# Performance work log

Hardware: AMD Instinct MI355X
Metric: run time of the kernel (lower is better)

The kernel has to match this reference:

```python
import jax, jax.numpy as jnp
import numpy as np

E = 1024      # emb_dim
H = 16        # num_heads
DH = E // H   # per-head atten_dim
B = 2
T = 2048


def _layernorm(x, scale, shift, eps=1e-5):
    mean = x.mean(axis=-1, keepdims=True)
    var = ((x - mean) ** 2).mean(axis=-1, keepdims=True)  # unbiased=False
    return scale * (x - mean) / jnp.sqrt(var + eps) + shift


def _gelu(x):
    # Faithful to source: tanh(sqrt(2/pi)*x + 0.044715*x^3)  (no sqrt on cubic term)
    c = jnp.sqrt(jnp.asarray(2.0 / jnp.pi, x.dtype))
    return 0.5 * x * (1.0 + jnp.tanh(c * x + 0.044715 * x ** 3))


def setup_inputs() -> dict:
    key = jax.random.key(0)
    ks = jax.random.split(key, 12)
    s = 0.02
    return {
        "x":     jax.random.normal(ks[0], (B, T, E), jnp.float32),
        "Wq":    jax.random.normal(ks[1], (H, E, DH), jnp.float32) * s,
        "Wk":    jax.random.normal(ks[2], (H, E, DH), jnp.float32) * s,
        "Wv":    jax.random.normal(ks[3], (H, E, DH), jnp.float32) * s,
        "fc_w":  jax.random.normal(ks[4], (E, E), jnp.float32) * s,
        "fc_b":  jnp.zeros((E,), jnp.float32),
        "ln1_s": jnp.ones((E,), jnp.float32),
        "ln1_b": jnp.zeros((E,), jnp.float32),
        "ln2_s": jnp.ones((E,), jnp.float32),
        "ln2_b": jnp.zeros((E,), jnp.float32),
        "ff_w1": jax.random.normal(ks[5], (E, 4 * E), jnp.float32) * s,
        "ff_b1": jnp.zeros((4 * E,), jnp.float32),
        "ff_w2": jax.random.normal(ks[6], (4 * E, E), jnp.float32) * s,
        "ff_b2": jnp.zeros((E,), jnp.float32),
    }


def _attention(x, Wq, Wk, Wv, fc_w, fc_b):
    b, t, _ = x.shape
    q = jnp.einsum("bte,hed->bhtd", x, Wq)
    k = jnp.einsum("bte,hed->bhtd", x, Wk)
    v = jnp.einsum("bte,hed->bhtd", x, Wv)
    scores = jnp.einsum("bhtd,bhsd->bhts", q, k)
    causal = jnp.triu(jnp.ones((t, t), bool), 1)
    scores = jnp.where(causal, -jnp.inf, scores)
    w = jax.nn.softmax(scores / jnp.sqrt(jnp.asarray(DH, x.dtype)), axis=-1)
    ctx = jnp.einsum("bhts,bhsd->bhtd", w, v)
    # faithful quirk from source: per-head transpose(1,2) then reshape(b, T, d_out)
    ctx = jnp.swapaxes(ctx, 2, 3).reshape(b, H, t, DH)
    concat = ctx.transpose(0, 2, 1, 3).reshape(b, t, E)
    return concat @ fc_w + fc_b


def reference(x, Wq, Wk, Wv, fc_w, fc_b, ln1_s, ln1_b, ln2_s, ln2_b,
              ff_w1, ff_b1, ff_w2, ff_b2):
    h = _attention(_layernorm(x, ln1_s, ln1_b), Wq, Wk, Wv, fc_w, fc_b) + x
    y = _layernorm(h, ln2_s, ln2_b)
    y = _gelu(y @ ff_w1 + ff_b1) @ ff_w2 + ff_b2
    return y + h
```

## Files before the change

### kernel.cpp

```cpp
#include <hip/hip_runtime.h>


#define En 1024
#define Hn 16
#define DHn 64
#define Bn 2
#define Tn 2048
#define Mrows 4096

typedef __attribute__((ext_vector_type(8))) short bf16x8;
typedef __attribute__((ext_vector_type(4))) float f32x4;

__device__ __forceinline__ short f2bf(float f) {
    unsigned u = __float_as_uint(f);
    u += 0x7FFFu + ((u >> 16) & 1u);
    return (short)(u >> 16);
}
__device__ __forceinline__ ushort f2bfu(float f) {
    unsigned u = __float_as_uint(f);
    u += 0x7FFFu + ((u >> 16) & 1u);
    return (ushort)(u >> 16);
}
__device__ __forceinline__ float bf2f(ushort u) {
    return __uint_as_float((unsigned)u << 16);
}

__device__ __forceinline__ float gelu_f(float x) {
    float u = 0.79788456080286535588f * x + 0.044715f * x * x * x;
    float t = __expf(2.0f * u);
    return x * t / (t + 1.0f);
}

__device__ __forceinline__ void load_lds16(const void* g, void* l) {
    __builtin_amdgcn_global_load_lds(
        (const __attribute__((address_space(1))) unsigned int*)(uintptr_t)g,
        (__attribute__((address_space(3))) unsigned int*)(uintptr_t)l,
        16, 0, 0);
}

__global__ __launch_bounds__(256) void ln_kernel(
    const float* __restrict__ in, const float* __restrict__ sc,
    const float* __restrict__ sh, ushort* __restrict__ out)
{
    int row = blockIdx.x;
    int tid = threadIdx.x;
    float4 v = ((const float4*)(in + (size_t)row * En))[tid];
    float s  = v.x + v.y + v.z + v.w;
    float s2 = v.x*v.x + v.y*v.y + v.z*v.z + v.w*v.w;
    #pragma unroll
    for (int off = 32; off > 0; off >>= 1) {
        s  += __shfl_down(s,  off);
        s2 += __shfl_down(s2, off);
    }
    __shared__ float red[2][4];
    int wave = tid >> 6, lane = tid & 63;
    if (lane == 0) { red[0][wave] = s; red[1][wave] = s2; }
    __syncthreads();
    s  = red[0][0] + red[0][1] + red[0][2] + red[0][3];
    s2 = red[1][0] + red[1][1] + red[1][2] + red[1][3];
    float mean = s * (1.0f / En);
    float var  = s2 * (1.0f / En) - mean * mean;
    float r = rsqrtf(var + 1e-5f);
    float4 scv = ((const float4*)sc)[tid];
    float4 shv = ((const float4*)sh)[tid];
    ushort4 o;
    o.x = f2bfu(scv.x * (v.x - mean) * r + shv.x);
    o.y = f2bfu(scv.y * (v.y - mean) * r + shv.y);
    o.z = f2bfu(scv.z * (v.z - mean) * r + shv.z);
    o.w = f2bfu(scv.w * (v.w - mean) * r + shv.w);
    ((ushort4*)(out + (size_t)row * En))[tid] = o;
}

__global__ __launch_bounds__(256) void ln2_fuse(
    const ushort* __restrict__ P0, const ushort* __restrict__ P1,
    const float* __restrict__ bias, const float* __restrict__ x,
    const float* __restrict__ sc, const float* __restrict__ sh,
    ushort* __restrict__ hb, ushort* __restrict__ ynb)
{
    int row = blockIdx.x, tid = threadIdx.x;
    size_t idx = (size_t)row * 256 + tid;
    ushort4 a = ((const ushort4*)P0)[idx];
    ushort4 b = ((const ushort4*)P1)[idx];
    float4 bi = ((const float4*)bias)[tid];
    float4 xr = ((const float4*)x)[idx];
    float4 v;
    v.x = bf2f(a.x) + bf2f(b.x) + bi.x + xr.x;
    v.y = bf2f(a.y) + bf2f(b.y) + bi.y + xr.y;
    v.z = bf2f(a.z) + bf2f(b.z) + bi.z + xr.z;
    v.w = bf2f(a.w) + bf2f(b.w) + bi.w + xr.w;
    ushort4 hv;
    hv.x = f2bfu(v.x); hv.y = f2bfu(v.y); hv.z = f2bfu(v.z); hv.w = f2bfu(v.w);
    ((ushort4*)hb)[idx] = hv;
    float s  = v.x + v.y + v.z + v.w;
    float s2 = v.x*v.x + v.y*v.y + v.z*v.z + v.w*v.w;
    #pragma unroll
    for (int off = 32; off > 0; off >>= 1) {
        s  += __shfl_down(s,  off);
        s2 += __shfl_down(s2, off);
    }
    __shared__ float red[2][4];
    int wave = tid >> 6, lane = tid & 63;
    if (lane == 0) { red[0][wave] = s; red[1][wave] = s2; }
    __syncthreads();
    s  = red[0][0] + red[0][1] + red[0][2] + red[0][3];
    s2 = red[1][0] + red[1][1] + red[1][2] + red[1][3];
    float mean = s * (1.0f / En);
    float var  = s2 * (1.0f / En) - mean * mean;
    float r = rsqrtf(var + 1e-5f);
    float4 scv = ((const float4*)sc)[tid];
    float4 shv = ((const float4*)sh)[tid];
    ushort4 o;
    o.x = f2bfu(scv.x * (v.x - mean) * r + shv.x);
    o.y = f2bfu(scv.y * (v.y - mean) * r + shv.y);
    o.z = f2bfu(scv.z * (v.z - mean) * r + shv.z);
    o.w = f2bfu(scv.w * (v.w - mean) * r + shv.w);
    ((ushort4*)ynb)[idx] = o;
}

__global__ __launch_bounds__(256) void ff2_reduce(
    const ushort* __restrict__ P0, const ushort* __restrict__ P1,
    const float* __restrict__ bias, const ushort* __restrict__ hb,
    float* __restrict__ out)
{
    int tid = threadIdx.x;
    size_t i = (size_t)blockIdx.x * 256 + tid;
    ushort4 a = ((const ushort4*)P0)[i];
    ushort4 b = ((const ushort4*)P1)[i];
    float4 bi = ((const float4*)bias)[tid];
    ushort4 hu = ((const ushort4*)hb)[i];
    float4 o;
    o.x = bf2f(a.x) + bf2f(b.x) + bi.x + bf2f(hu.x);
    o.y = bf2f(a.y) + bf2f(b.y) + bi.y + bf2f(hu.y);
    o.z = bf2f(a.z) + bf2f(b.z) + bi.z + bf2f(hu.z);
    o.w = bf2f(a.w) + bf2f(b.w) + bi.w + bf2f(hu.w);
    ((float4*)out)[i] = o;
}

__global__ __launch_bounds__(256) void prep_w(
    const float* __restrict__ Wq, const float* __restrict__ Wk,
    const float* __restrict__ Wv, const float* __restrict__ fc_w,
    const float* __restrict__ ff_w1, const float* __restrict__ ff_w2,
    ushort* __restrict__ wqkv, ushort* __restrict__ wfc,
    ushort* __restrict__ wf1, ushort* __restrict__ wf2)
{
    int bid = blockIdx.x;
    const float* in; ushort* out; int N, ldo, k0, n0;
    if (bid < 768) {
        int z = bid >> 4, kb = bid & 15;
        int sel = z / 16, h = z % 16;
        in  = (sel == 0 ? Wq : sel == 1 ? Wk : Wv) + (size_t)h * En * DHn;
        out = wqkv + (size_t)(sel * 1024 + h * 64) * En;
        N = DHn; ldo = En; k0 = kb * 64; n0 = 0;
    } else if (bid < 1024) {
        int b2 = bid - 768;
        in = fc_w; out = wfc; N = En; ldo = En;
        k0 = (b2 & 15) * 64; n0 = (b2 >> 4) * 64;
    } else if (bid < 2048) {
        int b2 = bid - 1024;
        in = ff_w1; out = wf1; N = 4 * En; ldo = En;
        k0 = (b2 & 15) * 64; n0 = (b2 >> 4) * 64;
    } else {
        int b2 = bid - 2048;
        in = ff_w2; out = wf2; N = En; ldo = 4 * En;
        k0 = (b2 & 63) * 64; n0 = (b2 >> 6) * 64;
    }
    __shared__ float t[64][65];
    int tid = threadIdx.x, r = tid >> 4, c4 = (tid & 15) * 4;
    #pragma unroll
    for (int i = 0; i < 4; ++i) {
        float4 v = *(const float4*)(in + (size_t)(k0 + r + i * 16) * N + n0 + c4);
        t[r + i * 16][c4 + 0] = v.x; t[r + i * 16][c4 + 1] = v.y;
        t[r + i * 16][c4 + 2] = v.z; t[r + i * 16][c4 + 3] = v.w;
    }
    __syncthreads();
    #pragma unroll
    for (int i = 0; i < 4; ++i) {
        int n = r + i * 16;
        ushort4 u;
        u.x = f2bfu(t[c4 + 0][n]); u.y = f2bfu(t[c4 + 1][n]);
        u.z = f2bfu(t[c4 + 2][n]); u.w = f2bfu(t[c4 + 3][n]);
        *(ushort4*)(out + (size_t)(n0 + n) * ldo + k0 + c4) = u;
    }
}

template<int MODE, int TN>
__global__ __launch_bounds__(256) void gemm_bf16(
    const ushort* __restrict__ A, int lda,
    const ushort* __restrict__ Bt, int ldb, int Kloop,
    const float* __restrict__ bias,
    ushort* __restrict__ Cb, int ldc,
    ushort* __restrict__ qo, ushort* __restrict__ ko, ushort* __restrict__ vo)
{
    constexpr int WCN = TN / 2;
    constexpr int NI  = WCN / 16;
    constexpr int BIW = TN * 8 / 256;
    constexpr int STAGE = 128 * 64 + TN * 64;
    constexpr int BOUNCE = (MODE == 2 || MODE == 1) ? 4 * 64 * 68
                         : (MODE == 3 ? 128 * 68 : 0);
    constexpr int SMEMN = STAGE > BOUNCE ? STAGE : BOUNCE;
    __shared__ ushort smem[SMEMN];
    ushort* As = smem;
    ushort* Bs = smem + 128 * 64;
    int tid = threadIdx.x, wv = tid >> 6, lid = tid & 63;
    int m0 = blockIdx.x * 128, n0 = blockIdx.y * TN;
    int koff = blockIdx.z * Kloop;
    int wr = wv >> 1, wc = wv & 1;
    int hm = lid & 15, hk = lid >> 4;

    f32x4 acc[4][NI];
    #pragma unroll
    for (int i = 0; i < 4; ++i)
        #pragma unroll
        for (int j = 0; j < NI; ++j) acc[i][j] = (f32x4){0.f, 0.f, 0.f, 0.f};

    const ushort* Abase = A + (size_t)m0 * lda + koff;
    const ushort* Bbase = Bt + (size_t)n0 * ldb + koff;

    for (int k0 = 0; k0 < Kloop; k0 += 64) {
        __syncthreads();
        #pragma unroll
        for (int i = 0; i < 4; ++i) {
            int c = wv * 256 + i * 64 + lid;
            int r = c >> 3, s = c & 7;
            int j = s ^ (r & 7);
            load_lds16(Abase + (size_t)r * lda + k0 + j * 8,
                       &As[(wv * 256 + i * 64) * 8]);
        }
        #pragma unroll
        for (int i = 0; i < BIW; ++i) {
            int c = wv * (BIW * 64) + i * 64 + lid;
            int r = c >> 3, s = c & 7;
            int j = s ^ (r & 7);
            load_lds16(Bbase + (size_t)r * ldb + k0 + j * 8,
                       &Bs[(wv * (BIW * 64) + i * 64) * 8]);
        }
        __syncthreads();
        #pragma unroll
        for (int kk = 0; kk < 2; ++kk) {
            bf16x8 af[4], bfr[NI];
            #pragma unroll
            for (int mi = 0; mi < 4; ++mi) {
                int r = wr * 64 + mi * 16 + hm;
                int slot = ((kk << 2) | hk) ^ (r & 7);
                af[mi] = *(const bf16x8*)&As[(r * 8 + slot) * 8];
            }
            #pragma unroll
            for (int ni = 0; ni < NI; ++ni) {
                int r = wc * WCN + ni * 16 + hm;
                int slot = ((kk << 2) | hk) ^ (r & 7);
                bfr[ni] = *(const bf16x8*)&Bs[(r * 8 + slot) * 8];
            }
            #pragma unroll
            for (int mi = 0; mi < 4; ++mi)
                #pragma unroll
                for (int ni = 0; ni < NI; ++ni)
                    acc[mi][ni] = __builtin_amdgcn_mfma_f32_16x16x32_bf16(
                        af[mi], bfr[ni], acc[mi][ni], 0, 0, 0);
        }
    }

    int colbase = n0 + wc * WCN + hm;
    int rowbase = m0 + wr * 64 + hk * 4;
    if (MODE == 1) {
        __syncthreads();
        ushort* Ls = smem + wv * (64 * 68);
        #pragma unroll
        for (int ni = 0; ni < NI; ++ni) {
            int col = colbase + ni * 16;
            float bb = bias[col];
            #pragma unroll
            for (int mi = 0; mi < 4; ++mi)
                #pragma unroll
                for (int r = 0; r < 4; ++r)
                    Ls[(mi * 16 + hk * 4 + r) * 68 + ni * 16 + hm] =
                        f2bfu(gelu_f(acc[mi][ni][r] + bb));
        }
        ushort* outp = Cb + (size_t)(m0 + wr * 64) * ldc + n0 + wc * 64;
        int dcol = hm * 4;
        #pragma unroll
        for (int i = 0; i < 16; ++i) {
            int t = hk + i * 4;
            *(ushort4*)(outp + (size_t)t * ldc + dcol) =
                *(const ushort4*)&Ls[t * 68 + dcol];
        }
    } else if (MODE == 2) {
        __syncthreads();
        ushort* Ls = smem + wv * (64 * 68);
        int col0 = n0 + wc * 64;
        int sel = col0 >> 10, h = (col0 & 1023) >> 6;
        if (sel < 2) {
            #pragma unroll
            for (int ni = 0; ni < NI; ++ni)
                #pragma unroll
                for (int mi = 0; mi < 4; ++mi)
                    #pragma unroll
                    for (int r = 0; r < 4; ++r)
                        Ls[(mi * 16 + hk * 4 + r) * 68 + ni * 16 + hm] =
                            f2bfu(acc[mi][ni][r]);
            ushort* outp = (sel == 0 ? qo : ko) + (size_t)h * (Mrows * DHn);
            int dcol = hm * 4;
            #pragma unroll
            for (int i = 0; i < 16; ++i) {
                int t = hk + i * 4;
                *(ushort4*)(outp + (size_t)(m0 + wr * 64 + t) * DHn + dcol) =
                    *(const ushort4*)&Ls[t * 68 + dcol];
            }
        } else {
            #pragma unroll
            for (int ni = 0; ni < NI; ++ni)
                #pragma unroll
                for (int mi = 0; mi < 4; ++mi)
                    #pragma unroll
                    for (int r = 0; r < 4; ++r)
                        Ls[(ni * 16 + hm) * 68 + mi * 16 + hk * 4 + r] =
                            f2bfu(acc[mi][ni][r]);
            int bb2 = m0 >> 11;
            int t0 = (m0 & 2047) + wr * 64;
            ushort* outp = vo + ((size_t)((h * 2 + bb2) * 64)) * Tn + t0;
            int tcol = hm * 4;
            #pragma unroll
            for (int i = 0; i < 16; ++i) {
                int d = hk + i * 4;
                *(ushort4*)(outp + (size_t)d * Tn + tcol) =
                    *(const ushort4*)&Ls[d * 68 + tcol];
            }
        }
    } else {
        __syncthreads();
        ushort* Ls = smem;
        #pragma unroll
        for (int ni = 0; ni < NI; ++ni)
            #pragma unroll
            for (int mi = 0; mi < 4; ++mi)
                #pragma unroll
                for (int r = 0; r < 4; ++r)
                    Ls[(wr * 64 + mi * 16 + hk * 4 + r) * 68
                       + wc * WCN + ni * 16 + hm] = f2bfu(acc[mi][ni][r]);
        __syncthreads();
        ushort* Cp = Cb + (size_t)blockIdx.z * Mrows * ldc;
        #pragma unroll
        for (int it = 0; it < 8; ++it) {
            int i = it * 1024 + tid * 4;
            int row = i >> 6, col = i & 63;
            *(ushort4*)(Cp + (size_t)(m0 + row) * ldc + n0 + col) =
                *(const ushort4*)&Ls[row * 68 + col];
        }
    }
}

__global__ __launch_bounds__(256) void attn_mfma(
    const ushort* __restrict__ q, const ushort* __restrict__ ksrc,
    const ushort* __restrict__ vtsrc, ushort* __restrict__ cat)
{
    int g = blockIdx.x;
    int h = g >> 1, b = g & 1;
    const ushort* qg  = q     + (size_t)g * Tn * DHn;
    const ushort* kg  = ksrc  + (size_t)g * Tn * DHn;
    const ushort* vtg = vtsrc + (size_t)g * DHn * Tn;
    int tid = threadIdx.x, wave = tid >> 6, lane = tid & 63;
    int m = lane & 15, gq = lane >> 4;

    __shared__ short Ks[4096];
    __shared__ short Vt[4096];
    __shared__ short Ps[4][1024];

    int R  = tid >> 2;
    int c2 = tid & 3;

    #pragma unroll 1
    for (int phase = 0; phase < 2; ++phase) {
        int qt = phase ? (31 - (int)blockIdx.y) : (int)blockIdx.y;
        int q0 = qt * 64;

        bf16x8 qf[2];
        {
            const ushort* qp = qg + (size_t)(q0 + wave * 16 + m) * DHn + gq * 8;
            qf[0] = *(const bf16x8*)(qp);
            qf[1] = *(const bf16x8*)(qp + 32);
        }
        f32x4 o[4];
        #pragma unroll
        for (int i = 0; i < 4; ++i) o[i] = (f32x4){0.f, 0.f, 0.f, 0.f};
        float lsum[4] = {0.f, 0.f, 0.f, 0.f};

        for (int kt = 0; kt <= qt; ++kt) {
            int k0 = kt * 64;
            __syncthreads();
            {
                const ushort* ksp = kg  + (size_t)(k0 + R) * DHn + c2 * 16;
                const ushort* vsp = vtg + (size_t)R * Tn + k0 + c2 * 16;
                bf16x8 f0 = *(const bf16x8*)(ksp);
                bf16x8 f1 = *(const bf16x8*)(ksp + 8);
                bf16x8 v0 = *(const bf16x8*)(vsp);
                bf16x8 v1 = *(const bf16x8*)(vsp + 8);
                *(bf16x8*)&Ks[R * 64 + (((c2 * 2    ) ^ (R & 7)) << 3)] = f0;
                *(bf16x8*)&Ks[R * 64 + (((c2 * 2 + 1) ^ (R & 7)) << 3)] = f1;
                *(bf16x8*)&Vt[R * 64 + (((c2 * 2    ) ^ (R & 7)) << 3)] = v0;
                *(bf16x8*)&Vt[R * 64 + (((c2 * 2 + 1) ^ (R & 7)) << 3)] = v1;
            }
            __syncthreads();

            bool diag = (kt == qt);
            float ps[4][4];
            #pragma unroll
            for (int ct = 0; ct < 4; ++ct) {
                if (diag && ct > wave) {
                    ps[ct][0] = ps[ct][1] = ps[ct][2] = ps[ct][3] = 0.f;
                    continue;
                }
                f32x4 acc = (f32x4){0.f, 0.f, 0.f, 0.f};
                int row = ct * 16 + m;
                #pragma unroll
                for (int db = 0; db < 2; ++db) {
                    bf16x8 kf = *(const bf16x8*)&Ks[row * 64 + (((db * 4 + gq) ^ (row & 7)) << 3)];
                    acc = __builtin_amdgcn_mfma_f32_16x16x32_bf16(qf[db], kf, acc, 0, 0, 0);
                }
                #pragma unroll
                for (int r = 0; r < 4; ++r) {
                    float p;
                    if (diag && (ct * 16 + m) > (wave * 16 + gq * 4 + r)) {
                        p = 0.f;
                    } else {
                        p = __expf(acc[r] * 0.125f);
                    }
                    ps[ct][r] = p;
                    lsum[r] += p;
                }
            }

            #pragma unroll
            for (int ct = 0; ct < 4; ++ct)
                #pragma unroll
                for (int r = 0; r < 4; ++r) {
                    int row = gq * 4 + r;
                    Ps[wave][row * 64 + ((((ct * 2 + (m >> 3)) ^ (row & 7)) << 3) | (m & 7))] =
                        f2bf(ps[ct][r]);
                }
            bf16x8 pf[2];
            #pragma unroll
            for (int db2 = 0; db2 < 2; ++db2)
                pf[db2] = *(const bf16x8*)&Ps[wave][m * 64 + (((db2 * 4 + gq) ^ (m & 7)) << 3)];

            #pragma unroll
            for (int ct2 = 0; ct2 < 4; ++ct2) {
                int row = ct2 * 16 + m;
                #pragma unroll
                for (int db2 = 0; db2 < 2; ++db2) {
                    bf16x8 vf = *(const bf16x8*)&Vt[row * 64 + (((db2 * 4 + gq) ^ (row & 7)) << 3)];
                    o[ct2] = __builtin_amdgcn_mfma_f32_16x16x32_bf16(pf[db2], vf, o[ct2], 0, 0, 0);
                }
            }
        }

        float inv[4];
        #pragma unroll
        for (int r = 0; r < 4; ++r) {
            float l = lsum[r];
            l += __shfl_xor(l, 1);
            l += __shfl_xor(l, 2);
            l += __shfl_xor(l, 4);
            l += __shfl_xor(l, 8);
            inv[r] = 1.0f / l;
        }
        size_t base = (size_t)b * Tn * En + (size_t)h * 64 + (size_t)qt * En
                    + wave * 16 + gq * 4;
        #pragma unroll
        for (int ct2 = 0; ct2 < 4; ++ct2) {
            int d = ct2 * 16 + m;
            #pragma unroll
            for (int r = 0; r < 4; ++r)
                cat[base + (size_t)d * 32 * En + r] = f2bfu(o[ct2][r] * inv[r]);
        }
    }
}

extern "C" void kernel_launch(void* const* d_in, const int* in_sizes, int n_in,
                              void* d_out, int out_size, void* d_ws, size_t ws_size,
                              hipStream_t stream) {
    const float* x     = (const float*)d_in[0];
    const float* Wq    = (const float*)d_in[1];
    const float* Wk    = (const float*)d_in[2];
    const float* Wv    = (const float*)d_in[3];
    const float* fc_w  = (const float*)d_in[4];
    const float* fc_b  = (const float*)d_in[5];
    const float* ln1_s = (const float*)d_in[6];
    const float* ln1_b = (const float*)d_in[7];
    const float* ln2_s = (const float*)d_in[8];
    const float* ln2_b = (const float*)d_in[9];
    const float* ff_w1 = (const float*)d_in[10];
    const float* ff_b1 = (const float*)d_in[11];
    const float* ff_w2 = (const float*)d_in[12];
    const float* ff_b2 = (const float*)d_in[13];
    float* out = (float*)d_out;
    (void)in_sizes; (void)n_in; (void)out_size; (void)ws_size;

    const size_t MB = 1048576;
    char* w8 = (char*)d_ws;
    ushort* S0   = (ushort*)(w8 + 0 * MB);
    ushort* kb   = (ushort*)(w8 + 8 * MB);
    ushort* vtb  = (ushort*)(w8 + 16 * MB);
    ushort* qb   = (ushort*)(w8 + 24 * MB);
    ushort* hb   = (ushort*)(w8 + 32 * MB);
    ushort* Pfc  = (ushort*)(w8 + 48 * MB);
    ushort* y1   = (ushort*)(w8 + 48 * MB);
    ushort* Pff2 = (ushort*)(w8 + 0 * MB);
    ushort* wqkv = (ushort*)(w8 + 80 * MB);
    ushort* wfc  = (ushort*)(w8 + 86 * MB);
    ushort* wf1  = (ushort*)(w8 + 88 * MB);
    ushort* wf2  = (ushort*)(w8 + 96 * MB);

    prep_w<<<dim3(3072), 256, 0, stream>>>(
        Wq, Wk, Wv, fc_w, ff_w1, ff_w2, wqkv, wfc, wf1, wf2);

    ln_kernel<<<dim3(Mrows), 256, 0, stream>>>(x, ln1_s, ln1_b, S0);
    gemm_bf16<2, 128><<<dim3(32, 24), 256, 0, stream>>>(
        S0, En, wqkv, En, En, nullptr, nullptr, 0, qb, kb, vtb);
    attn_mfma<<<dim3(Hn * Bn, 16), 256, 0, stream>>>(qb, kb, vtb, S0);
    gemm_bf16<3, 64><<<dim3(32, 16, 2), 256, 0, stream>>>(
        S0, En, wfc, En, En / 2, nullptr, Pfc, En, nullptr, nullptr, nullptr);
    ln2_fuse<<<dim3(Mrows), 256, 0, stream>>>(
        Pfc, Pfc + (size_t)Mrows * En, fc_b, x, ln2_s, ln2_b, hb, qb);
    gemm_bf16<1, 128><<<dim3(32, 32), 256, 0, stream>>>(
        qb, En, wf1, En, En, ff_b1, y1, 4 * En, nullptr, nullptr, nullptr);
    gemm_bf16<3, 64><<<dim3(32, 16, 2), 256, 0, stream>>>(
        y1, 4 * En, wf2, 4 * En, 2 * En, nullptr, Pff2, En, nullptr, nullptr, nullptr);
    ff2_reduce<<<dim3(Mrows), 256, 0, stream>>>(
        Pff2, Pff2 + (size_t)Mrows * En, ff_b2, hb, out);
}
```

Before: 346.3 us.

## Add 256x256 tiled 8-wave GEMM kernel with staged LDS pipelining for QKV/FF GEMMs

Adds a new 512-thread GEMM kernel that computes 256x256 output tiles. It double-buffers LDS through direct global-to-LDS loads split into phases, uses XOR-swizzled LDS layouts, and raises MFMA priority around the compute phases. The QKV, FF1 and FF2 GEMMs now use it, and FF2 switches from a split-K of 2 to a split-K of 4, with a matching four-way reduce kernel. The aim is more data reuse per tile and better overlap of loads with MFMA work. The cost is fewer blocks, which may leave CUs idle, plus extra partial-sum traffic from the deeper split-K.

```diff
diff --git a/kernel.cpp b/kernel.cpp
--- a/kernel.cpp
+++ b/kernel.cpp
@@ -117,22 +117,24 @@
     ((ushort4*)ynb)[idx] = o;
 }
 
-__global__ __launch_bounds__(256) void ff2_reduce(
-    const ushort* __restrict__ P0, const ushort* __restrict__ P1,
-    const float* __restrict__ bias, const ushort* __restrict__ hb,
-    float* __restrict__ out)
+__global__ __launch_bounds__(256) void ff2_reduce4(
+    const ushort* __restrict__ P, const float* __restrict__ bias,
+    const ushort* __restrict__ hb, float* __restrict__ out)
 {
     int tid = threadIdx.x;
     size_t i = (size_t)blockIdx.x * 256 + tid;
-    ushort4 a = ((const ushort4*)P0)[i];
-    ushort4 b = ((const ushort4*)P1)[i];
+    const size_t S = (size_t)Mrows * En / 4;
+    ushort4 a = ((const ushort4*)P)[i];
+    ushort4 b = ((const ushort4*)P)[i + S];
+    ushort4 c = ((const ushort4*)P)[i + 2 * S];
+    ushort4 d = ((const ushort4*)P)[i + 3 * S];
     float4 bi = ((const float4*)bias)[tid];
     ushort4 hu = ((const ushort4*)hb)[i];
     float4 o;
-    o.x = bf2f(a.x) + bf2f(b.x) + bi.x + bf2f(hu.x);
-    o.y = bf2f(a.y) + bf2f(b.y) + bi.y + bf2f(hu.y);
-    o.z = bf2f(a.z) + bf2f(b.z) + bi.z + bf2f(hu.z);
-    o.w = bf2f(a.w) + bf2f(b.w) + bi.w + bf2f(hu.w);
+    o.x = (bf2f(a.x) + bf2f(b.x)) + (bf2f(c.x) + bf2f(d.x)) + bi.x + bf2f(hu.x);
+    o.y = (bf2f(a.y) + bf2f(b.y)) + (bf2f(c.y) + bf2f(d.y)) + bi.y + bf2f(hu.y);
+    o.z = (bf2f(a.z) + bf2f(b.z)) + (bf2f(c.z) + bf2f(d.z)) + bi.z + bf2f(hu.z);
+    o.w = (bf2f(a.w) + bf2f(b.w)) + (bf2f(c.w) + bf2f(d.w)) + bi.w + bf2f(hu.w);
     ((float4*)out)[i] = o;
 }
 
@@ -348,6 +350,223 @@
     }
 }
 
+#define PHASE_MID() do { \
+    __builtin_amdgcn_s_barrier(); \
+    asm volatile("s_waitcnt lgkmcnt(0)" ::: "memory"); \
+    __builtin_amdgcn_sched_barrier(0); \
+} while (0)
+
+#define LOAD_AF(MH, KK) \
+    _Pragma("unroll") \
+    for (int mi = 0; mi < 4; ++mi) { \
+        int r = wr * 128 + (MH) * 64 + mi * 16 + hm; \
+        af[mi] = *(const bf16x8*)&As_[(r * 8 + ((((KK) << 2) | hk) ^ (r & 7))) * 8]; \
+    }
+
+#define MFMA_PHASE(MH, KK) do { \
+    __builtin_amdgcn_s_setprio(1); \
+    _Pragma("unroll") \
+    for (int mi = 0; mi < 4; ++mi) \
+        _Pragma("unroll") \
+        for (int ni = 0; ni < 4; ++ni) \
+            acc[(MH) * 4 + mi][ni] = __builtin_amdgcn_mfma_f32_16x16x32_bf16( \
+                af[mi], bfr[KK][ni], acc[(MH) * 4 + mi][ni], 0, 0, 0); \
+    __builtin_amdgcn_s_setprio(0); \
+} while (0)
+
+#define STAGE_A(bufp, h, ksrc) do { \
+    ushort* _d = smem + (bufp) * 32768; \
+    load_lds16(Abase + aoff[h][0] + (ksrc), _d + ldsoff[h][0]); \
+    load_lds16(Abase + aoff[h][1] + (ksrc), _d + ldsoff[h][1]); \
+} while (0)
+
+#define STAGE_B(bufp, h, ksrc) do { \
+    ushort* _d = smem + (bufp) * 32768 + 16384; \
+    load_lds16(Bbase + boff[h][0] + (ksrc), _d + ldsoff[h][0]); \
+    load_lds16(Bbase + boff[h][1] + (ksrc), _d + ldsoff[h][1]); \
+} while (0)
+
+template<int MODE>
+__global__ __launch_bounds__(512, 2) void gemm256(
+    const ushort* __restrict__ A, int lda,
+    const ushort* __restrict__ Bt, int ldb, int Kloop,
+    const float* __restrict__ bias,
+    ushort* __restrict__ Cb, int ldc,
+    ushort* __restrict__ qo, ushort* __restrict__ ko, ushort* __restrict__ vo)
+{
+    __shared__ ushort smem[65536];
+    int tid = threadIdx.x, wv = tid >> 6, lid = tid & 63;
+    int wr = wv >> 2, wc = wv & 3;
+    int hm = lid & 15, hk = lid >> 4;
+    int m0 = blockIdx.x * 256, n0 = blockIdx.y * 256;
+    int koff = blockIdx.z * Kloop;
+    int NT = Kloop >> 6;
+
+    const ushort* Abase = A + (size_t)m0 * lda + koff;
+    const ushort* Bbase = Bt + (size_t)n0 * ldb + koff;
+
+    int aoff[2][2], boff[2][2], ldsoff[2][2];
+    #pragma unroll
+    for (int h = 0; h < 2; ++h)
+        #pragma unroll
+        for (int i = 0; i < 2; ++i) {
+            int c = h * 1024 + wv * 128 + i * 64 + lid;
+            int r = c >> 3, s = c & 7, j = s ^ (r & 7);
+            aoff[h][i] = r * lda + j * 8;
+            boff[h][i] = r * ldb + j * 8;
+            ldsoff[h][i] = (h * 1024 + wv * 128 + i * 64) * 8;
+        }
+
+    f32x4 acc[8][4];
+    #pragma unroll
+    for (int i = 0; i < 8; ++i)
+        #pragma unroll
+        for (int j = 0; j < 4; ++j) acc[i][j] = (f32x4){0.f, 0.f, 0.f, 0.f};
+
+    STAGE_A(0, 0, 0); STAGE_A(0, 1, 0);
+    STAGE_B(0, 0, 0); STAGE_B(0, 1, 0);
+    {
+        int k1 = (NT > 1 ? 1 : 0) << 6;
+        STAGE_B(1, 0, k1); STAGE_B(1, 1, k1);
+    }
+    asm volatile("s_waitcnt vmcnt(4)" ::: "memory");
+    __builtin_amdgcn_s_barrier();
+
+    for (int t = 0; t < NT; ++t) {
+        int cur = t & 1, nxt = cur ^ 1;
+        int kA = (t + 1 < NT ? t + 1 : NT - 1) << 6;
+        int kB = (t + 2 < NT ? t + 2 : NT - 1) << 6;
+        const ushort* As_ = smem + cur * 32768;
+        const ushort* Bs_ = As_ + 16384;
+        bf16x8 af[4], bfr[2][4];
+
+        LOAD_AF(0, 0);
+        #pragma unroll
+        for (int kk = 0; kk < 2; ++kk)
+            #pragma unroll
+            for (int ni = 0; ni < 4; ++ni) {
+                int r = wc * 64 + ni * 16 + hm;
+                bfr[kk][ni] = *(const bf16x8*)
+                    &Bs_[(r * 8 + (((kk << 2) | hk) ^ (r & 7))) * 8];
+            }
+        STAGE_A(nxt, 0, kA);
+        PHASE_MID();
+        MFMA_PHASE(0, 0);
+        __builtin_amdgcn_s_barrier();
+
+        LOAD_AF(1, 0);
+        STAGE_A(nxt, 1, kA);
+        PHASE_MID();
+        MFMA_PHASE(1, 0);
+        __builtin_amdgcn_s_barrier();
+
+        LOAD_AF(0, 1);
+        STAGE_B(cur, 0, kB);
+        PHASE_MID();
+        MFMA_PHASE(0, 1);
+        __builtin_amdgcn_s_barrier();
+
+        LOAD_AF(1, 1);
+        STAGE_B(cur, 1, kB);
+        PHASE_MID();
+        MFMA_PHASE(1, 1);
+        asm volatile("s_waitcnt vmcnt(4)" ::: "memory");
+        __builtin_amdgcn_s_barrier();
+    }
+    asm volatile("s_waitcnt vmcnt(0)" ::: "memory");
+    __builtin_amdgcn_s_barrier();
+
+    ushort* Ls = smem + wv * (64 * 68);
+    int dcol = hm * 4;
+    if (MODE == 1) {
+        float bb[4];
+        #pragma unroll
+        for (int ni = 0; ni < 4; ++ni) bb[ni] = bias[n0 + wc * 64 + ni * 16 + hm];
+        #pragma unroll
+        for (int mh = 0; mh < 2; ++mh) {
+            #pragma unroll
+            for (int ni = 0; ni < 4; ++ni)
+                #pragma unroll
+                for (int mi = 0; mi < 4; ++mi)
+                    #pragma unroll
+                    for (int r = 0; r < 4; ++r)
+                        Ls[(mi * 16 + hk * 4 + r) * 68 + ni * 16 + hm] =
+                            f2bfu(gelu_f(acc[mh * 4 + mi][ni][r] + bb[ni]));
+            ushort* outp = Cb + (size_t)(m0 + wr * 128 + mh * 64) * ldc
+                              + n0 + wc * 64;
+            #pragma unroll
+            for (int i = 0; i < 16; ++i) {
+                int tt = hk + i * 4;
+                *(ushort4*)(outp + (size_t)tt * ldc + dcol) =
+                    *(const ushort4*)&Ls[tt * 68 + dcol];
+            }
+        }
+    } else if (MODE == 2) {
+        int col0 = n0 + wc * 64;
+        int sel = col0 >> 10, hh = (col0 & 1023) >> 6;
+        #pragma unroll
+        for (int mh = 0; mh < 2; ++mh) {
+            int rowb = m0 + wr * 128 + mh * 64;
+            if (sel < 2) {
+                #pragma unroll
+                for (int ni = 0; ni < 4; ++ni)
+                    #pragma unroll
+                    for (int mi = 0; mi < 4; ++mi)
+                        #pragma unroll
+                        for (int r = 0; r < 4; ++r)
+                            Ls[(mi * 16 + hk * 4 + r) * 68 + ni * 16 + hm] =
+                                f2bfu(acc[mh * 4 + mi][ni][r]);
+                ushort* outp = (sel == 0 ? qo : ko) + (size_t)hh * (Mrows * DHn);
+                #pragma unroll
+                for (int i = 0; i < 16; ++i) {
+                    int tt = hk + i * 4;
+                    *(ushort4*)(outp + (size_t)(rowb + tt) * DHn + dcol) =
+                        *(const ushort4*)&Ls[tt * 68 + dcol];
+                }
+            } else {
+                #pragma unroll
+                for (int ni = 0; ni < 4; ++ni)
+                    #pragma unroll
+                    for (int mi = 0; mi < 4; ++mi)
+                        #pragma unroll
+                        for (int r = 0; r < 4; ++r)
+                            Ls[(ni * 16 + hm) * 68 + mi * 16 + hk * 4 + r] =
+                                f2bfu(acc[mh * 4 + mi][ni][r]);
+                int bb2 = m0 >> 11;
+                int t0 = (m0 & 2047) + wr * 128 + mh * 64;
+                ushort* outp = vo + ((size_t)((hh * 2 + bb2) * 64)) * Tn + t0;
+                #pragma unroll
+                for (int i = 0; i < 16; ++i) {
+                    int d = hk + i * 4;
+                    *(ushort4*)(outp + (size_t)d * Tn + dcol) =
+                        *(const ushort4*)&Ls[d * 68 + dcol];
+                }
+            }
+        }
+    } else {
+        ushort* Cp = Cb + (size_t)blockIdx.z * ((size_t)Mrows * ldc);
+        #pragma unroll
+        for (int mh = 0; mh < 2; ++mh) {
+            #pragma unroll
+            for (int ni = 0; ni < 4; ++ni)
+                #pragma unroll
+                for (int mi = 0; mi < 4; ++mi)
+                    #pragma unroll
+                    for (int r = 0; r < 4; ++r)
+                        Ls[(mi * 16 + hk * 4 + r) * 68 + ni * 16 + hm] =
+                            f2bfu(acc[mh * 4 + mi][ni][r]);
+            ushort* outp = Cp + (size_t)(m0 + wr * 128 + mh * 64) * ldc
+                              + n0 + wc * 64;
+            #pragma unroll
+            for (int i = 0; i < 16; ++i) {
+                int tt = hk + i * 4;
+                *(ushort4*)(outp + (size_t)tt * ldc + dcol) =
+                    *(const ushort4*)&Ls[tt * 68 + dcol];
+            }
+        }
+    }
+}
+
 __global__ __launch_bounds__(256) void attn_mfma(
     const ushort* __restrict__ q, const ushort* __restrict__ ksrc,
     const ushort* __restrict__ vtsrc, ushort* __restrict__ cat)
@@ -513,17 +732,16 @@
         Wq, Wk, Wv, fc_w, ff_w1, ff_w2, wqkv, wfc, wf1, wf2);
 
     ln_kernel<<<dim3(Mrows), 256, 0, stream>>>(x, ln1_s, ln1_b, S0);
-    gemm_bf16<2, 128><<<dim3(32, 24), 256, 0, stream>>>(
+    gemm256<2><<<dim3(16, 12), 512, 0, stream>>>(
         S0, En, wqkv, En, En, nullptr, nullptr, 0, qb, kb, vtb);
     attn_mfma<<<dim3(Hn * Bn, 16), 256, 0, stream>>>(qb, kb, vtb, S0);
     gemm_bf16<3, 64><<<dim3(32, 16, 2), 256, 0, stream>>>(
         S0, En, wfc, En, En / 2, nullptr, Pfc, En, nullptr, nullptr, nullptr);
     ln2_fuse<<<dim3(Mrows), 256, 0, stream>>>(
         Pfc, Pfc + (size_t)Mrows * En, fc_b, x, ln2_s, ln2_b, hb, qb);
-    gemm_bf16<1, 128><<<dim3(32, 32), 256, 0, stream>>>(
+    gemm256<1><<<dim3(16, 16), 512, 0, stream>>>(
         qb, En, wf1, En, En, ff_b1, y1, 4 * En, nullptr, nullptr, nullptr);
-    gemm_bf16<3, 64><<<dim3(32, 16, 2), 256, 0, stream>>>(
-        y1, 4 * En, wf2, 4 * En, 2 * En, nullptr, Pff2, En, nullptr, nullptr, nullptr);
-    ff2_reduce<<<dim3(Mrows), 256, 0, stream>>>(
-        Pff2, Pff2 + (size_t)Mrows * En, ff_b2, hb, out);
-}
+    gemm256<3><<<dim3(16, 4, 4), 512, 0, stream>>>(
+        y1, 4 * En, wf2, 4 * En, En, nullptr, Pff2, En, nullptr, nullptr, nullptr);
+    ff2_reduce4<<<dim3(Mrows), 256, 0, stream>>>(Pff2, ff_b2, hb, out);
+}
```

Result: faster. 330.5 us (-4.6%).
